# Optimization experiments

Measured on AMD Instinct MI355X. Metric: run time of the kernel, lower is better.

The kernel has to match this reference:

```python
import jax, jax.numpy as jnp
import numpy as np

ATTENTION_DIM = 256
TEMPERATURE = 1.0
NEG_INF = -2.0**32 + 1.0  # matches tf code's padding value


def setup_inputs() -> dict:
    key = jax.random.key(0)
    k1, k2, k3, k4, k5, k6, k7 = jax.random.split(key, 7)
    B, Q, M, QD, MD, AD, VD = 8, 2048, 2048, 512, 512, 256, 256
    inputs = jax.random.normal(k1, (B, Q, QD), dtype=jnp.float32)
    memory = jax.random.normal(k2, (B, M, MD), dtype=jnp.float32)
    memory_lengths = jnp.maximum(jax.random.randint(k3, (B,), 0, M + 1), 1).astype(jnp.int32)
    query_lengths = jnp.maximum(jax.random.randint(k4, (B,), 0, Q + 1), 1).astype(jnp.int32)
    s = 0.02
    Wq = jax.random.normal(k5, (QD, AD), dtype=jnp.float32) * s
    Wk = jax.random.normal(k6, (MD, AD), dtype=jnp.float32) * s
    Wv = jax.random.normal(k7, (MD, VD), dtype=jnp.float32) * s
    return {"inputs": inputs, "memory": memory, "memory_lengths": memory_lengths,
            "query_lengths": query_lengths, "Wq": Wq, "Wk": Wk, "Wv": Wv}


def reference(inputs, memory, memory_lengths, query_lengths, Wq, Wk, Wv):
    # Dense projections (no bias). NOTE: original code (faithfully reproduced)
    # computes values with the KEY layer; Wv is unused.
    queries = jnp.einsum('bqd,da->bqa', inputs, Wq)   # [B,Q,AD]
    keys = jnp.einsum('bmd,da->bma', memory, Wk)      # [B,M,AD]
    values = jnp.einsum('bmd,da->bma', memory, Wk)    # [B,M,AD] (bug in source)

    logits = jnp.einsum('bqa,bma->bqm', queries, keys)
    logits = logits / jnp.sqrt(jnp.float32(ATTENTION_DIM)) / TEMPERATURE

    B, Q, _ = inputs.shape
    M = memory.shape[1]
    mem_mask = jnp.arange(M)[None, :] < memory_lengths[:, None]   # [B,M]
    qry_mask = jnp.arange(Q)[None, :] < query_lengths[:, None]    # [B,Q]
    length_mask = qry_mask[:, :, None] & mem_mask[:, None, :]     # [B,Q,M]

    logits = jnp.where(length_mask, logits, jnp.float32(NEG_INF))
    alignments = jax.nn.softmax(logits, axis=2)                   # [B,Q,M]
    contexts = jnp.einsum('bqm,bma->bqa', alignments, values)     # [B,Q,AD]
    return contexts, alignments
```

## Files before the change

kernel.cpp:

```cpp
#include <hip/hip_runtime.h>
#include <hip/hip_bf16.h>

typedef __attribute__((ext_vector_type(8))) short s8v;
typedef __attribute__((ext_vector_type(4))) float f4v;
typedef __attribute__((ext_vector_type(4))) unsigned short us4;
typedef unsigned short u16;

__device__ __forceinline__ u16 f2bf(float f) {
  union { float f; unsigned int u; } x;
  x.f = f;
  unsigned int lsb = (x.u >> 16) & 1u;
  return (u16)((x.u + 0x7fffu + lsb) >> 16);
}

__device__ __forceinline__ float bf2f(u16 u) {
  union { unsigned int i; float f; } x;
  x.i = ((unsigned int)u) << 16;
  return x.f;
}

__device__ __forceinline__ uint4 pack8(float4 a, float4 b) {
  union { u16 u[8]; uint4 v; } t;
  t.u[0] = f2bf(a.x); t.u[1] = f2bf(a.y); t.u[2] = f2bf(a.z); t.u[3] = f2bf(a.w);
  t.u[4] = f2bf(b.x); t.u[5] = f2bf(b.y); t.u[6] = f2bf(b.z); t.u[7] = f2bf(b.w);
  return t.v;
}

__global__ __launch_bounds__(256) void proj_kernel(
    const float* __restrict__ inputs, const float* __restrict__ memory,
    const float* __restrict__ Wq, const float* __restrict__ Wk,
    u16* __restrict__ qb, u16* __restrict__ krow, u16* __restrict__ kcol)
{
  __shared__ u16 Wt[64 * 264];
  __shared__ u16 At[64 * 40];

  const int tid = threadIdx.x;
  const int w = tid >> 6;
  const int l = tid & 63;
  const int lr = l & 15;
  const int lh = l >> 4;
  const int rbase = blockIdx.x * 64;
  const int n0 = blockIdx.y * 64;
  const int src = blockIdx.z;
  const float* __restrict__ A  = src ? memory : inputs;
  const float* __restrict__ Wg = src ? Wk : Wq;

  f4v acc[4];
#pragma unroll
  for (int i = 0; i < 4; ++i) acc[i] = f4v{0.f, 0.f, 0.f, 0.f};

  for (int kh = 0; kh < 2; ++kh) {
    {
      const int kl = tid >> 3;
      const int nl = (tid & 7) * 8;
#pragma unroll
      for (int i = 0; i < 8; ++i) {
        const int k = kl + i * 32;
        const float* s = Wg + (size_t)(kh * 256 + k) * 256 + n0 + nl;
        float4 x0 = *(const float4*)s;
        float4 x1 = *(const float4*)(s + 4);
        Wt[(nl + 0) * 264 + k] = f2bf(x0.x);
        Wt[(nl + 1) * 264 + k] = f2bf(x0.y);
        Wt[(nl + 2) * 264 + k] = f2bf(x0.z);
        Wt[(nl + 3) * 264 + k] = f2bf(x0.w);
        Wt[(nl + 4) * 264 + k] = f2bf(x1.x);
        Wt[(nl + 5) * 264 + k] = f2bf(x1.y);
        Wt[(nl + 6) * 264 + k] = f2bf(x1.z);
        Wt[(nl + 7) * 264 + k] = f2bf(x1.w);
      }
    }
    __syncthreads();
    for (int ks = 0; ks < 8; ++ks) {
      {
        const int row = tid >> 2;
        const int kk = (tid & 3) * 8;
        const float* s = A + (size_t)(rbase + row) * 512 + kh * 256 + ks * 32 + kk;
        float4 x0 = *(const float4*)s;
        float4 x1 = *(const float4*)(s + 4);
        *(uint4*)&At[row * 40 + kk] = pack8(x0, x1);
      }
      __syncthreads();
      const s8v af = *(const s8v*)&At[(w * 16 + lr) * 40 + lh * 8];
#pragma unroll
      for (int nt = 0; nt < 4; ++nt) {
        const s8v bf = *(const s8v*)&Wt[(nt * 16 + lr) * 264 + ks * 32 + lh * 8];
        acc[nt] = __builtin_amdgcn_mfma_f32_16x16x32_bf16(af, bf, acc[nt], 0, 0, 0);
      }
      __syncthreads();
    }
  }

  u16* __restrict__ dst = src ? krow : qb;
#pragma unroll
  for (int nt = 0; nt < 4; ++nt) {
    const int col = n0 + nt * 16 + lr;
    const int R0 = rbase + w * 16 + lh * 4;
    u16 u0 = f2bf(acc[nt][0]);
    u16 u1 = f2bf(acc[nt][1]);
    u16 u2 = f2bf(acc[nt][2]);
    u16 u3 = f2bf(acc[nt][3]);
    dst[(size_t)(R0 + 0) * 256 + col] = u0;
    dst[(size_t)(R0 + 1) * 256 + col] = u1;
    dst[(size_t)(R0 + 2) * 256 + col] = u2;
    dst[(size_t)(R0 + 3) * 256 + col] = u3;
    if (src) {
      const int bb = R0 >> 11;
      const int mm = R0 & 2047;
      us4 pk;
      pk[0] = u0; pk[1] = u1; pk[2] = u2; pk[3] = u3;
      *(us4*)&kcol[((size_t)bb * 256 + col) * 2048 + mm] = pk;
    }
  }
}

__global__ __launch_bounds__(256) void attn_sum_kernel(
    const u16* __restrict__ qb, const u16* __restrict__ krow,
    const int* __restrict__ mlens, const int* __restrict__ qlens,
    float* __restrict__ psum_p, u16* __restrict__ pb)
{
  __shared__ u16 kr[32 * 264];
  __shared__ u16 pl[4 * 16 * 40];

  const int tid = threadIdx.x;
  const int w = tid >> 6;
  const int l = tid & 63;
  const int lr = l & 15;
  const int lh = l >> 4;
  const int b = blockIdx.y;
  const int q0 = blockIdx.x * 64;
  const int ms = blockIdx.z;
  const int m_base = ms * 512;
  const int mlen = mlens[b];
  const int qlen = qlens[b];
  const int qrow0 = q0 + w * 16 + lh * 4;

  s8v qf[8];
  {
    const u16* qp = qb + ((size_t)b * 2048 + q0 + w * 16 + lr) * 256 + lh * 8;
#pragma unroll
    for (int s = 0; s < 8; ++s) qf[s] = *(const s8v*)(qp + s * 32);
  }

  float psum[4] = {0.f, 0.f, 0.f, 0.f};
  const float C2 = 0.09016844005556021f;

  for (int mo = 0; mo < 512; mo += 32) {
    const int m0 = m_base + mo;
#pragma unroll
    for (int i = 0; i < 4; ++i) {
      const int idx = i * 256 + tid;
      const int m = idx >> 5, G = idx & 31;
      uint4 v = *(const uint4*)(krow + (((size_t)b * 2048 + m0 + m) << 8) + G * 8);
      *(uint4*)&kr[m * 264 + G * 8] = v;
    }
    __syncthreads();

    f4v sacc[2];
    sacc[0] = f4v{0.f, 0.f, 0.f, 0.f};
    sacc[1] = f4v{0.f, 0.f, 0.f, 0.f};
#pragma unroll
    for (int s = 0; s < 8; ++s) {
#pragma unroll
      for (int f = 0; f < 2; ++f) {
        const s8v bf = *(const s8v*)&kr[(f * 16 + lr) * 264 + s * 32 + lh * 8];
        sacc[f] = __builtin_amdgcn_mfma_f32_16x16x32_bf16(qf[s], bf, sacc[f], 0, 0, 0);
      }
    }

#pragma unroll
    for (int f = 0; f < 2; ++f) {
      const int m = m0 + f * 16 + lr;
      const bool vm = m < mlen;
#pragma unroll
      for (int r = 0; r < 4; ++r) {
        float p = exp2f(sacc[f][r] * C2);
        if (!vm) p = 0.f;
        if (qrow0 + r >= qlen) p = 1.f;
        psum[r] += p;
        pl[w * 640 + (lh * 4 + r) * 40 + f * 16 + lr] = f2bf(p);
      }
    }

    const s8v pav = *(const s8v*)&pl[w * 640 + lr * 40 + lh * 8];
    *(s8v*)(pb + ((size_t)b * 2048 + q0 + w * 16 + lr) * 2048 + m0 + lh * 8) = pav;
    __syncthreads();
  }

#pragma unroll
  for (int r = 0; r < 4; ++r) {
    float v = psum[r];
    v += __shfl_xor(v, 1);
    v += __shfl_xor(v, 2);
    v += __shfl_xor(v, 4);
    v += __shfl_xor(v, 8);
    psum[r] = v;
  }
  if (lr == 0) {
#pragma unroll
    for (int r = 0; r < 4; ++r)
      psum_p[ms * 16384 + b * 2048 + qrow0 + r] = psum[r];
  }
}

__global__ __launch_bounds__(256) void pv_kernel(
    const u16* __restrict__ pb, const u16* __restrict__ kcol,
    const float* __restrict__ psum_p, float* __restrict__ out_align,
    float* __restrict__ out_ctx, float* __restrict__ octx_ws)
{
  __shared__ u16 kc[256 * 40];

  const int tid = threadIdx.x;
  const int w = tid >> 6;
  const int wq = w >> 1;
  const int wa = w & 1;
  const int l = tid & 63;
  const int lr = l & 15;
  const int lh = l >> 4;
  const int b = blockIdx.y;
  const int qb32 = blockIdx.x * 32;
  const int mh = blockIdx.z;
  const int mstart = (mh == 0) ? 0 : (mh == 1 ? 704 : 1376);
  const int mcount = (mh == 0) ? 704 : 672;

  const int qa = qb32 + wq * 16 + lr;
  float inv_a;
  {
    const int q = b * 2048 + qa;
    inv_a = 1.0f / (psum_p[q] + psum_p[16384 + q] + psum_p[32768 + q] + psum_p[49152 + q]);
  }
  float inv_c[4];
#pragma unroll
  for (int r = 0; r < 4; ++r) {
    const int q = b * 2048 + qb32 + wq * 16 + lh * 4 + r;
    inv_c[r] = 1.0f / (psum_p[q] + psum_p[16384 + q] + psum_p[32768 + q] + psum_p[49152 + q]);
  }

  f4v oacc[8];
#pragma unroll
  for (int i = 0; i < 8; ++i) oacc[i] = f4v{0.f, 0.f, 0.f, 0.f};

  for (int mo = 0; mo < mcount; mo += 32) {
    const int m0 = mstart + mo;
#pragma unroll
    for (int i = 0; i < 4; ++i) {
      const int idx = i * 256 + tid;
      const int a2 = idx >> 2, gm = idx & 3;
      uint4 v2 = *(const uint4*)(kcol + (((size_t)b * 256 + a2) << 11) + m0 + gm * 8);
      *(uint4*)&kc[a2 * 40 + gm * 8] = v2;
    }
    __syncthreads();

    const s8v pa = *(const s8v*)(pb + ((size_t)b * 2048 + qa) * 2048 + m0 + lh * 8);

    if (wa == 0) {
      f4v f0, f1;
      f0[0] = bf2f((u16)pa[0]) * inv_a; f0[1] = bf2f((u16)pa[1]) * inv_a;
      f0[2] = bf2f((u16)pa[2]) * inv_a; f0[3] = bf2f((u16)pa[3]) * inv_a;
      f1[0] = bf2f((u16)pa[4]) * inv_a; f1[1] = bf2f((u16)pa[5]) * inv_a;
      f1[2] = bf2f((u16)pa[6]) * inv_a; f1[3] = bf2f((u16)pa[7]) * inv_a;
      float* ap = out_align + ((size_t)b * 2048 + qa) * 2048 + m0 + lh * 8;
      __builtin_nontemporal_store(f0, (f4v*)ap);
      __builtin_nontemporal_store(f1, (f4v*)(ap + 4));
    }

#pragma unroll
    for (int at = 0; at < 8; ++at) {
      const s8v vf = *(const s8v*)&kc[(wa * 128 + at * 16 + lr) * 40 + lh * 8];
      oacc[at] = __builtin_amdgcn_mfma_f32_16x16x32_bf16(pa, vf, oacc[at], 0, 0, 0);
    }
    __syncthreads();
  }

  float* __restrict__ dst = (mh == 0) ? out_ctx : (octx_ws + (size_t)(mh - 1) * 4194304);
#pragma unroll
  for (int at = 0; at < 8; ++at) {
    const int a = wa * 128 + at * 16 + lr;
#pragma unroll
    for (int r = 0; r < 4; ++r) {
      __builtin_nontemporal_store(oacc[at][r] * inv_c[r],
          &dst[((size_t)b * 2048 + qb32 + wq * 16 + lh * 4 + r) * 256 + a]);
    }
  }
}

__global__ __launch_bounds__(256) void combine_kernel(
    float* __restrict__ out_ctx, const float* __restrict__ octx_ws)
{
  const size_t i = (size_t)blockIdx.x * 256 + threadIdx.x;
  float4 a = ((const float4*)out_ctx)[i];
  float4 c0 = ((const float4*)octx_ws)[i];
  float4 c1 = ((const float4*)(octx_ws + 4194304))[i];
  a.x += c0.x + c1.x; a.y += c0.y + c1.y;
  a.z += c0.z + c1.z; a.w += c0.w + c1.w;
  ((float4*)out_ctx)[i] = a;
}

extern "C" void kernel_launch(void* const* d_in, const int* in_sizes, int n_in,
                              void* d_out, int out_size, void* d_ws, size_t ws_size,
                              hipStream_t stream) {
  const float* inputs = (const float*)d_in[0];
  const float* memory = (const float*)d_in[1];
  const int* mlens    = (const int*)d_in[2];
  const int* qlens    = (const int*)d_in[3];
  const float* Wq     = (const float*)d_in[4];
  const float* Wk     = (const float*)d_in[5];
  (void)in_sizes; (void)n_in; (void)out_size; (void)ws_size;

  u16* wsu = (u16*)d_ws;
  u16* qb   = wsu;
  u16* krow = wsu + 4194304;
  u16* kcol = wsu + 8388608;
  float* psum_p = (float*)(wsu + 12582912);
  u16* pbuf = wsu + 12713984;
  float* octx_ws = (float*)(wsu + 46268416);

  float* out_ctx = (float*)d_out;
  float* out_align = out_ctx + 4194304;

  proj_kernel<<<dim3(256, 4, 2), dim3(256), 0, stream>>>(
      inputs, memory, Wq, Wk, qb, krow, kcol);
  attn_sum_kernel<<<dim3(32, 8, 4), dim3(256), 0, stream>>>(
      qb, krow, mlens, qlens, psum_p, pbuf);
  pv_kernel<<<dim3(64, 8, 3), dim3(256), 0, stream>>>(
      pbuf, kcol, psum_p, out_align, out_ctx, octx_ws);
  combine_kernel<<<dim3(4096), dim3(256), 0, stream>>>(out_ctx, octx_ws);
}
```

Baseline: 189.3 us.

## Load K/V MFMA operands directly from global memory, drop LDS staging and barriers

Both the score kernel and the PV kernel stop staging K/V tiles into shared memory. Each wave now reads its MFMA B-operands straight from global memory (through L1/L2), which removes two __syncthreads per iteration. The probability-buffer store and load become nontemporal. This trades LDS traffic and barrier stalls for redundant global loads across waves, and those loads may be less coalesced and higher latency.

Result: slower. 402.1 us (+112.4%).

```diff
diff --git a/kernel.cpp b/kernel.cpp
--- a/kernel.cpp
+++ b/kernel.cpp
@@ -118,7 +118,6 @@
     const int* __restrict__ mlens, const int* __restrict__ qlens,
     float* __restrict__ psum_p, u16* __restrict__ pb)
 {
-  __shared__ u16 kr[32 * 264];
   __shared__ u16 pl[4 * 16 * 40];
 
   const int tid = threadIdx.x;
@@ -143,17 +142,10 @@
 
   float psum[4] = {0.f, 0.f, 0.f, 0.f};
   const float C2 = 0.09016844005556021f;
+  const u16* __restrict__ kb = krow + (size_t)b * 2048 * 256;
 
   for (int mo = 0; mo < 512; mo += 32) {
     const int m0 = m_base + mo;
-#pragma unroll
-    for (int i = 0; i < 4; ++i) {
-      const int idx = i * 256 + tid;
-      const int m = idx >> 5, G = idx & 31;
-      uint4 v = *(const uint4*)(krow + (((size_t)b * 2048 + m0 + m) << 8) + G * 8);
-      *(uint4*)&kr[m * 264 + G * 8] = v;
-    }
-    __syncthreads();
 
     f4v sacc[2];
     sacc[0] = f4v{0.f, 0.f, 0.f, 0.f};
@@ -162,7 +154,7 @@
     for (int s = 0; s < 8; ++s) {
 #pragma unroll
       for (int f = 0; f < 2; ++f) {
-        const s8v bf = *(const s8v*)&kr[(f * 16 + lr) * 264 + s * 32 + lh * 8];
+        const s8v bf = *(const s8v*)(kb + (size_t)(m0 + f * 16 + lr) * 256 + s * 32 + lh * 8);
         sacc[f] = __builtin_amdgcn_mfma_f32_16x16x32_bf16(qf[s], bf, sacc[f], 0, 0, 0);
       }
     }
@@ -182,8 +174,8 @@
     }
 
     const s8v pav = *(const s8v*)&pl[w * 640 + lr * 40 + lh * 8];
-    *(s8v*)(pb + ((size_t)b * 2048 + q0 + w * 16 + lr) * 2048 + m0 + lh * 8) = pav;
-    __syncthreads();
+    __builtin_nontemporal_store(pav,
+        (s8v*)(pb + ((size_t)b * 2048 + q0 + w * 16 + lr) * 2048 + m0 + lh * 8));
   }
 
 #pragma unroll
@@ -207,8 +199,6 @@
     const float* __restrict__ psum_p, float* __restrict__ out_align,
     float* __restrict__ out_ctx, float* __restrict__ octx_ws)
 {
-  __shared__ u16 kc[256 * 40];
-
   const int tid = threadIdx.x;
   const int w = tid >> 6;
   const int wq = w >> 1;
@@ -239,18 +229,13 @@
 #pragma unroll
   for (int i = 0; i < 8; ++i) oacc[i] = f4v{0.f, 0.f, 0.f, 0.f};
 
+  const u16* __restrict__ prow = pb + ((size_t)b * 2048 + qa) * 2048;
+  const u16* __restrict__ vbase = kcol + ((size_t)b * 256 + wa * 128) * 2048;
+
   for (int mo = 0; mo < mcount; mo += 32) {
     const int m0 = mstart + mo;
-#pragma unroll
-    for (int i = 0; i < 4; ++i) {
-      const int idx = i * 256 + tid;
-      const int a2 = idx >> 2, gm = idx & 3;
-      uint4 v2 = *(const uint4*)(kcol + (((size_t)b * 256 + a2) << 11) + m0 + gm * 8);
-      *(uint4*)&kc[a2 * 40 + gm * 8] = v2;
-    }
-    __syncthreads();
-
-    const s8v pa = *(const s8v*)(pb + ((size_t)b * 2048 + qa) * 2048 + m0 + lh * 8);
+
+    const s8v pa = __builtin_nontemporal_load((const s8v*)(prow + m0 + lh * 8));
 
     if (wa == 0) {
       f4v f0, f1;
@@ -265,10 +250,9 @@
 
 #pragma unroll
     for (int at = 0; at < 8; ++at) {
-      const s8v vf = *(const s8v*)&kc[(wa * 128 + at * 16 + lr) * 40 + lh * 8];
+      const s8v vf = *(const s8v*)(vbase + (size_t)(at * 16 + lr) * 2048 + m0 + lh * 8);
       oacc[at] = __builtin_amdgcn_mfma_f32_16x16x32_bf16(pa, vf, oacc[at], 0, 0, 0);
     }
-    __syncthreads();
   }
 
   float* __restrict__ dst = (mh == 0) ? out_ctx : (octx_ws + (size_t)(mh - 1) * 4194304);
```
